# Performance work log

Measured on AMD Instinct MI355X. Metric: run time of the kernel, lower is better.

Reference implementation:

```python
import jax, jax.numpy as jnp
import numpy as np
from jax import lax

B, C, H, W = 2, 64, 128, 128
F_SCALE, STRIDE = 2, 2
F = F_SCALE * STRIDE            # pixel-unshuffle factor = 4
CK = C // 16                    # attention channel dim = 4
SCALE_DIM = C // F_SCALE        # softmax scale uses embed_size//f_scale = 32


def setup_inputs() -> dict:
    key = jax.random.key(0)
    ks = jax.random.split(key, 16)
    g = lambda i, shape, s=0.05: jax.random.normal(ks[i], shape, jnp.float32) * s
    return {
        "x":   jax.random.normal(ks[0], (B, C, H, W), jnp.float32),
        # conv1 = Sequential(1x1 C->CK, 1x1 CK->CK)
        "w1a": g(1, (CK, C)), "b1a": g(2, (CK,)),
        "w1b": g(3, (CK, CK)), "b1b": g(4, (CK,)),
        # wqk parameter (torch.randn, std 1)
        "wqk": jax.random.normal(ks[5], (CK, CK), jnp.float32),
        # conv2: 1x1 CK->C ; conv: 1x1 C->C
        "w2":  g(6, (C, CK)), "b2": g(7, (C,)),
        "wc":  g(8, (C, C)), "bc": g(9, (C,)),
        # FF (GridSANaive): 1x1 C->C/4, 3x3 dilated C/4->C/4, 1x1 C/4->C
        "wf1": g(10, (C // 4, C)), "bf1": g(11, (C // 4,)),
        "wf2": g(12, (C // 4, C // 4, 3, 3)), "bf2": g(13, (C // 4,)),
        "wf3": g(14, (C, C // 4)), "bf3": g(15, (C,)),
    }


def conv1x1(x, w, b):
    return jnp.einsum('bchw,oc->bohw', x, w) + b[None, :, None, None]


def grid_attention(x, wqk):
    b, c, h, w = x.shape
    sh = h // 2
    x = jnp.pad(x, ((0, 0), (0, 0), (sh, 0), (0, 0)))      # Shift2d pad (top)
    # F.layer_norm over last 3 dims, no affine, eps=1e-5
    mu = jnp.mean(x, axis=(1, 2, 3), keepdims=True)
    var = jnp.var(x, axis=(1, 2, 3), keepdims=True)
    xx = (x - mu) / jnp.sqrt(var + 1e-5)
    hh, ww = xx.shape[2], xx.shape[3]
    ph, pw = (F - hh % F) % F, (F - ww % F) % F
    xx = jnp.pad(xx, ((0, 0), (0, 0), (0, ph), (0, pw)))
    gh, gw = (hh + ph) // F, (ww + pw) // F
    # pixel_unshuffle: channel layout (c, fy, fx)
    xx = xx.reshape(b, c, gh, F, gw, F).transpose(0, 1, 3, 5, 2, 4)
    xx = xx.reshape(b, c * F * F, gh, gw)
    # rearrange 'b (f c) h w -> (b f) c h w', f=F*F (mixes layout, as in original)
    xx = xx.reshape(b * F * F, c, gh, gw)
    L = gh * gw
    tok = xx.transpose(0, 2, 3, 1).reshape(b * F * F, L, c)   # (bg, L, c)
    qk = tok @ wqk
    qk = qk / (jnp.linalg.norm(qk, axis=-1, keepdims=True) + 1e-8)
    attn = (jnp.einsum('blk,bmk->blm', qk, qk) + 1.0) / (SCALE_DIM ** 0.5)
    attn = jax.nn.softmax(attn, axis=-1)
    out = jnp.einsum('blm,bmc->blc', attn, tok)
    out = out.reshape(b * F * F, gh, gw, c).transpose(0, 3, 1, 2)
    out = out.reshape(b, F * F * c, gh, gw)
    # pixel_shuffle: channel layout (fy, fx, c)
    out = out.reshape(b, F, F, c, gh, gw).transpose(0, 3, 4, 1, 5, 2)
    out = out.reshape(b, c, gh * F, gw * F)
    out = out[:, :, :hh, :ww]                               # undo shuffle pad
    return out[:, :, :-sh, :] if sh > 0 else out            # Shift2d crop (bottom)


def ff(x, wf1, bf1, wf2, bf2, wf3, bf3):
    h1 = jax.nn.relu(conv1x1(x, wf1, bf1))
    k = 1 + (STRIDE // 2) * 2   # ShiftConv2d offset for 3x3, dilation=STRIDE
    hp = jnp.pad(h1, ((0, 0), (0, 0), (k, 0), (0, 0)))
    h2 = lax.conv_general_dilated(
        hp, wf2, (1, 1), ((STRIDE, STRIDE), (STRIDE, STRIDE)),
        rhs_dilation=(STRIDE, STRIDE),
        dimension_numbers=('NCHW', 'OIHW', 'NCHW'))
    h2 = jax.nn.relu((h2 + bf2[None, :, None, None])[:, :, :-k, :])
    return conv1x1(h2, wf3, bf3)


def reference(x, w1a, b1a, w1b, b1b, wqk, w2, b2, wc, bc,
              wf1, bf1, wf2, bf2, wf3, bf3):
    a = conv1x1(conv1x1(x, w1a, b1a), w1b, b1b)
    att = grid_attention(a, wqk)
    y = x + conv1x1(conv1x1(att, w2, b2), wc, bc)
    return y + ff(y, wf1, bf1, wf2, bf2, wf3, bf3)
```

## Files before the change

### kernel.cpp

```cpp
#include <hip/hip_runtime.h>
#include <math.h>

#define CHW  (64*16384)
#define ATT_SCALE 0.17677669529663687f

__global__ __launch_bounds__(256) void k1_a_stats(
    const float* __restrict__ x, const float* __restrict__ w1a,
    const float* __restrict__ b1a, const float* __restrict__ w1b,
    const float* __restrict__ b1b, float* __restrict__ a,
    float* __restrict__ statsbuf) {
  __shared__ float sA[256];
  __shared__ float sb1[4];
  __shared__ float pc[4][4][256];
  __shared__ float rs[64], rq[64];
  int tid = threadIdx.x;
  {
    int o = tid >> 6, c = tid & 63;
    float s = 0.f;
    #pragma unroll
    for (int k = 0; k < 4; ++k) s += w1b[o*4+k] * w1a[k*64+c];
    sA[tid] = s;
  }
  if (tid < 4) {
    float s = b1b[tid];
    #pragma unroll
    for (int k = 0; k < 4; ++k) s += w1b[tid*4+k] * b1a[k];
    sb1[tid] = s;
  }
  __syncthreads();
  int quad = tid & 15, cg = tid >> 4;
  int gq = blockIdx.x * 16 + quad;
  int bb = gq >> 12;
  int px0 = (gq & 4095) * 4;
  const float* xp = x + bb*CHW + (cg*4)*16384 + px0;
  float4 acc[4];
  #pragma unroll
  for (int o = 0; o < 4; ++o) acc[o] = make_float4(0.f,0.f,0.f,0.f);
  #pragma unroll
  for (int cc = 0; cc < 4; ++cc) {
    float4 xv = *(const float4*)(xp + cc*16384);
    int c = cg*4 + cc;
    #pragma unroll
    for (int o = 0; o < 4; ++o) {
      float w = sA[o*64+c];
      acc[o].x += w*xv.x; acc[o].y += w*xv.y; acc[o].z += w*xv.z; acc[o].w += w*xv.w;
    }
  }
  #pragma unroll
  for (int o = 0; o < 4; ++o) {
    pc[0][o][tid] = acc[o].x; pc[1][o][tid] = acc[o].y;
    pc[2][o][tid] = acc[o].z; pc[3][o][tid] = acc[o].w;
  }
  __syncthreads();
  if (tid < 64) {
    int q2 = tid & 15, o = tid >> 4;
    float sx=0.f, sy=0.f, sz=0.f, sw=0.f;
    #pragma unroll
    for (int g2 = 0; g2 < 16; ++g2) {
      int idx = g2*16 + q2;
      sx += pc[0][o][idx]; sy += pc[1][o][idx];
      sz += pc[2][o][idx]; sw += pc[3][o][idx];
    }
    float bv = sb1[o];
    sx += bv; sy += bv; sz += bv; sw += bv;
    int gq2 = blockIdx.x*16 + q2;
    int b2 = gq2 >> 12; int p0 = (gq2 & 4095)*4;
    *(float4*)(a + b2*4*16384 + o*16384 + p0) = make_float4(sx,sy,sz,sw);
    rs[tid] = sx+sy+sz+sw;
    rq[tid] = sx*sx+sy*sy+sz*sz+sw*sw;
  }
  __syncthreads();
  for (int s2 = 32; s2; s2 >>= 1) {
    if (tid < s2) { rs[tid] += rs[tid+s2]; rq[tid] += rq[tid+s2]; }
    __syncthreads();
  }
  if (tid == 0) { statsbuf[blockIdx.x*2] = rs[0]; statsbuf[blockIdx.x*2+1] = rq[0]; }
}

__device__ __forceinline__ float poly_exp(float d) {
  return 1.f + d*(1.f + d*(0.5f + d*(0.16666667f + d*0.04166667f)));
}
__global__ __launch_bounds__(512) void k3_attn(
    const float* __restrict__ a, const float* __restrict__ statsbuf,
    const float* __restrict__ wqk, float* __restrict__ att) {
  __shared__ float4 kq[1024];
  __shared__ float4 kt[1024];
  __shared__ float red[16][5][128];
  __shared__ float sred[8];
  int tid = threadIdx.x;
  int g = blockIdx.x >> 3, qb = blockIdx.x & 7;
  int b = g >> 4, u = (g >> 2) & 3, v = g & 3;

  if (tid < 256) {
    float2 p = ((const float2*)statsbuf)[b*256 + tid];
    float vs = p.x, vq = p.y;
    #pragma unroll
    for (int off = 32; off; off >>= 1) {
      vs += __shfl_down(vs, off); vq += __shfl_down(vq, off);
    }
    if ((tid & 63) == 0) { sred[tid>>6] = vs; sred[4 + (tid>>6)] = vq; }
  }
  __syncthreads();
  float mu  = (sred[0]+sred[1]+sred[2]+sred[3]) * (1.f/98304.f);
  float var = (sred[4]+sred[5]+sred[6]+sred[7]) * (1.f/98304.f) - mu*mu;
  float rsig = rsqrtf(var + 1e-5f);

  const float* ap = a + (b*4+u)*16384;
  for (int m = tid; m < 1024; m += 512) {
    int t = 512 + m;
    int i = t >> 5, j = m & 31;
    float4 tv = *(const float4*)(ap + (i*4 + v - 64)*128 + j*4);
    tv.x = (tv.x-mu)*rsig; tv.y = (tv.y-mu)*rsig;
    tv.z = (tv.z-mu)*rsig; tv.w = (tv.w-mu)*rsig;
    float q0 = tv.x*wqk[0] + tv.y*wqk[4] + tv.z*wqk[8]  + tv.w*wqk[12];
    float q1 = tv.x*wqk[1] + tv.y*wqk[5] + tv.z*wqk[9]  + tv.w*wqk[13];
    float q2 = tv.x*wqk[2] + tv.y*wqk[6] + tv.z*wqk[10] + tv.w*wqk[14];
    float q3 = tv.x*wqk[3] + tv.y*wqk[7] + tv.z*wqk[11] + tv.w*wqk[15];
    float inv = 1.f / (sqrtf(q0*q0 + q1*q1 + q2*q2 + q3*q3) + 1e-8f);
    kq[m] = make_float4(q0*inv, q1*inv, q2*inv, q3*inv);
    kt[m] = tv;
  }
  float z = -mu*rsig;
  float4 t0tv = make_float4(z, z, z, z);
  float p0 = z*(wqk[0] + wqk[4] + wqk[8]  + wqk[12]);
  float p1 = z*(wqk[1] + wqk[5] + wqk[9]  + wqk[13]);
  float p2 = z*(wqk[2] + wqk[6] + wqk[10] + wqk[14]);
  float p3 = z*(wqk[3] + wqk[7] + wqk[11] + wqk[15]);
  float inv0 = 1.f / (sqrtf(p0*p0 + p1*p1 + p2*p2 + p3*p3) + 1e-8f);
  float4 t0qk = make_float4(p0*inv0, p1*inv0, p2*inv0, p3*inv0);
  __syncthreads();

  if (qb >= 4) {
    int qi = tid & 31, s = tid >> 5;
    int t0 = (qb - 4)*128 + qi*4;
    float4 q[4];
    #pragma unroll
    for (int j = 0; j < 4; ++j) {
      float4 vq = kq[t0 + j];
      q[j] = make_float4(vq.x*ATT_SCALE, vq.y*ATT_SCALE, vq.z*ATT_SCALE, vq.w*ATT_SCALE);
    }
    float den[4] = {0.f,0.f,0.f,0.f};
    float4 ov[4];
    #pragma unroll
    for (int j = 0; j < 4; ++j) ov[j] = make_float4(0.f,0.f,0.f,0.f);
    if (s == 0) {
      #pragma unroll
      for (int j = 0; j < 4; ++j) {
        float d = q[j].x*t0qk.x + q[j].y*t0qk.y + q[j].z*t0qk.z + q[j].w*t0qk.w;
        float e = 512.f * poly_exp(d);
        den[j] += e;
        ov[j].x += e*t0tv.x; ov[j].y += e*t0tv.y; ov[j].z += e*t0tv.z; ov[j].w += e*t0tv.w;
      }
    }
    int m0 = s * 64;
    #pragma unroll 2
    for (int m = m0; m < m0 + 64; ++m) {
      float4 kk = kq[m];
      float4 tv = kt[m];
      #pragma unroll
      for (int j = 0; j < 4; ++j) {
        float d = q[j].x*kk.x + q[j].y*kk.y + q[j].z*kk.z + q[j].w*kk.w;
        float e = poly_exp(d);
        den[j] += e;
        ov[j].x += e*tv.x; ov[j].y += e*tv.y; ov[j].z += e*tv.z; ov[j].w += e*tv.w;
      }
    }
    #pragma unroll
    for (int j = 0; j < 4; ++j) {
      int key = j*32 + qi;
      red[s][0][key] = den[j];
      red[s][1][key] = ov[j].x; red[s][2][key] = ov[j].y;
      red[s][3][key] = ov[j].z; red[s][4][key] = ov[j].w;
    }
    __syncthreads();
    if (tid < 128) {
      int qi_r = tid & 31, j_r = tid >> 5;
      float dsum=0.f, ox=0.f, oy=0.f, oz=0.f, ow=0.f;
      #pragma unroll
      for (int ss = 0; ss < 16; ++ss) {
        dsum += red[ss][0][tid];
        ox += red[ss][1][tid]; oy += red[ss][2][tid];
        oz += red[ss][3][tid]; ow += red[ss][4][tid];
      }
      float inv = 1.f / dsum;
      int t = qb*128 + qi_r*4 + j_r;
      int i = t >> 5, j = t & 31;
      float* ap2 = att + b*4*16384 + (i*4+u)*128 + (j*4+v);
      ap2[0]     = ox*inv;
      ap2[16384] = oy*inv;
      ap2[32768] = oz*inv;
      ap2[49152] = ow*inv;
    }
  } else {
    float4 qs = make_float4(t0qk.x*ATT_SCALE, t0qk.y*ATT_SCALE,
                            t0qk.z*ATT_SCALE, t0qk.w*ATT_SCALE);
    float den = 0.f; float4 ov = make_float4(0.f,0.f,0.f,0.f);
    #pragma unroll
    for (int mm = 0; mm < 2; ++mm) {
      int m = tid*2 + mm;
      float4 kk = kq[m];
      float4 tv = kt[m];
      float d = qs.x*kk.x + qs.y*kk.y + qs.z*kk.z + qs.w*kk.w;
      float e = poly_exp(d);
      den += e;
      ov.x += e*tv.x; ov.y += e*tv.y; ov.z += e*tv.z; ov.w += e*tv.w;
    }
    if (tid == 0) {
      float d = qs.x*t0qk.x + qs.y*t0qk.y + qs.z*t0qk.z + qs.w*t0qk.w;
      float e = 512.f * poly_exp(d);
      den += e;
      ov.x += e*t0tv.x; ov.y += e*t0tv.y; ov.z += e*t0tv.z; ov.w += e*t0tv.w;
    }
    float* sc = &red[0][0][0];
    sc[tid]        = den;
    sc[512 + tid]  = ov.x;
    sc[1024 + tid] = ov.y;
    sc[1536 + tid] = ov.z;
    sc[2048 + tid] = ov.w;
    __syncthreads();
    for (int s2 = 256; s2; s2 >>= 1) {
      if (tid < s2) {
        sc[tid]        += sc[tid + s2];
        sc[512 + tid]  += sc[512 + tid + s2];
        sc[1024 + tid] += sc[1024 + tid + s2];
        sc[1536 + tid] += sc[1536 + tid + s2];
        sc[2048 + tid] += sc[2048 + tid + s2];
      }
      __syncthreads();
    }
    float invd = 1.f / sc[0];
    float res0 = sc[512]*invd, res1 = sc[1024]*invd,
          res2 = sc[1536]*invd, res3 = sc[2048]*invd;
    int comp = tid >> 7, tloc = tid & 127;
    int t = qb*128 + tloc;
    int i = t >> 5, j = t & 31;
    float val = (comp == 0) ? res0 : (comp == 1) ? res1 : (comp == 2) ? res2 : res3;
    att[b*4*16384 + comp*16384 + (i*4+u)*128 + (j*4+v)] = val;
  }
}

__global__ __launch_bounds__(512) void k46_row(
    const float* __restrict__ x, const float* __restrict__ att,
    const float* __restrict__ w2p, const float* __restrict__ b2p,
    const float* __restrict__ wcp, const float* __restrict__ bcp,
    const float* __restrict__ wf1, const float* __restrict__ bf1,
    const float* __restrict__ wf2, const float* __restrict__ bf2,
    const float* __restrict__ wf3, const float* __restrict__ bf3,
    float* __restrict__ yo) {
  __shared__ float sWf[64][4];
  __shared__ float sbf[64];
  __shared__ float sw1[1024];
  __shared__ float sb1[16];
  __shared__ float4 satt[4][32];
  __shared__ float4 ylds[64][32];
  __shared__ float sbuf[16][3][136];
  __shared__ float h2buf[128][21];
  int tid = threadIdx.x;
  int lid = (blockIdx.x & 7) * 32 + (blockIdx.x >> 3);
  int bb = lid >> 7, h = lid & 127;

  if (tid < 256) {
    int o = tid >> 2, k = tid & 3;
    float s = 0.f;
    for (int c = 0; c < 64; ++c) s += wcp[o*64+c] * w2p[c*4+k];
    sWf[o][k] = s;
  }
  if (tid < 64) {
    float s = bcp[tid];
    for (int c = 0; c < 64; ++c) s += wcp[tid*64+c] * b2p[c];
    sbf[tid] = s;
  }
  for (int i = tid; i < 1024; i += 512) sw1[i] = wf1[i];
  if (tid < 16) sb1[tid] = bf1[tid];
  for (int idx = tid; idx < 16*3*136; idx += 512) (&sbuf[0][0][0])[idx] = 0.f;

  int quad = tid & 31, og = tid >> 5;
  #pragma unroll 1
  for (int ri = 0; ri < 4; ++ri) {
    int row = (ri == 3) ? h : (h - 5 + 2*ri);
    bool valid = (row >= 0);
    __syncthreads();
    if (valid && tid < 128) {
      int k = tid >> 5, q2 = tid & 31;
      satt[k][q2] = *(const float4*)(att + bb*4*16384 + k*16384 + row*128 + q2*4);
    }
    __syncthreads();
    if (valid) {
      float4 a0 = satt[0][quad], a1 = satt[1][quad],
             a2 = satt[2][quad], a3 = satt[3][quad];
      const float* xp = x + bb*CHW + row*128 + quad*4;
      #pragma unroll
      for (int cc = 0; cc < 4; ++cc) {
        int c = og*4 + cc;
        float4 xv = *(const float4*)(xp + c*16384);
        float w0 = sWf[c][0], w1 = sWf[c][1], w2v = sWf[c][2], w3 = sWf[c][3];
        float bv = sbf[c];
        float4 yv;
        yv.x = xv.x + w0*a0.x + w1*a1.x + w2v*a2.x + w3*a3.x + bv;
        yv.y = xv.y + w0*a0.y + w1*a1.y + w2v*a2.y + w3*a3.y + bv;
        yv.z = xv.z + w0*a0.z + w1*a1.z + w2v*a2.z + w3*a3.z + bv;
        yv.w = xv.w + w0*a0.w + w1*a1.w + w2v*a2.w + w3*a3.w + bv;
        ylds[c][quad] = yv;
      }
    }
    __syncthreads();
    if (valid && ri < 3) {
      float bv = sb1[og];
      float4 acc = make_float4(bv, bv, bv, bv);
      #pragma unroll 8
      for (int c = 0; c < 64; ++c) {
        float4 yv = ylds[c][quad];
        float wa = sw1[og*64+c];
        acc.x += wa*yv.x; acc.y += wa*yv.y; acc.z += wa*yv.z; acc.w += wa*yv.w;
      }
      int col = 4 + quad*4;
      sbuf[og][ri][col]   = fmaxf(acc.x, 0.f);
      sbuf[og][ri][col+1] = fmaxf(acc.y, 0.f);
      sbuf[og][ri][col+2] = fmaxf(acc.z, 0.f);
      sbuf[og][ri][col+3] = fmaxf(acc.w, 0.f);
    }
  }
  __syncthreads();

  int w = tid & 127;
  int g = __builtin_amdgcn_readfirstlane(tid >> 7);
  float acc[4];
  #pragma unroll
  for (int o = 0; o < 4; ++o) acc[o] = bf2[g*4+o];
  #pragma unroll 4
  for (int c = 0; c < 16; ++c) {
    #pragma unroll
    for (int r = 0; r < 3; ++r) {
      float tm2 = sbuf[c][r][w+2];
      float t00 = sbuf[c][r][w+4];
      float tp2 = sbuf[c][r][w+6];
      #pragma unroll
      for (int o = 0; o < 4; ++o) {
        const float* wp = wf2 + (((g*4+o)*16 + c)*3 + r)*3;
        acc[o] += wp[0]*tm2 + wp[1]*t00 + wp[2]*tp2;
      }
    }
  }
  #pragma unroll
  for (int o = 0; o < 4; ++o) h2buf[w][g*4+o] = fmaxf(acc[o], 0.f);
  __syncthreads();
  float hv[16];
  #pragma unroll
  for (int k = 0; k < 16; ++k) hv[k] = h2buf[w][k];
  const float* yrow = (const float*)ylds;
  float* ybase = yo + bb*CHW + h*128 + w;
  #pragma unroll 4
  for (int oc = 0; oc < 16; ++oc) {
    int o = g*16 + oc;
    float sv = bf3[o] + yrow[o*128 + w];
    #pragma unroll
    for (int k = 0; k < 16; ++k) sv += wf3[o*16+k]*hv[k];
    ybase[o*16384] = sv;
  }
}

extern "C" void kernel_launch(void* const* d_in, const int* in_sizes, int n_in,
                              void* d_out, int out_size, void* d_ws, size_t ws_size,
                              hipStream_t stream) {
  (void)in_sizes; (void)n_in; (void)out_size; (void)ws_size;
  const float* x   = (const float*)d_in[0];
  const float* w1a = (const float*)d_in[1];
  const float* b1a = (const float*)d_in[2];
  const float* w1b = (const float*)d_in[3];
  const float* b1b = (const float*)d_in[4];
  const float* wqk = (const float*)d_in[5];
  const float* w2  = (const float*)d_in[6];
  const float* b2  = (const float*)d_in[7];
  const float* wc  = (const float*)d_in[8];
  const float* bc  = (const float*)d_in[9];
  const float* wf1 = (const float*)d_in[10];
  const float* bf1 = (const float*)d_in[11];
  const float* wf2 = (const float*)d_in[12];
  const float* bf2 = (const float*)d_in[13];
  const float* wf3 = (const float*)d_in[14];
  const float* bf3 = (const float*)d_in[15];

  float* ws = (float*)d_ws;
  float*  a_    = ws;
  float*  stats = ws + 131072;
  float*  att   = ws + 525312;

  k1_a_stats<<<512, 256, 0, stream>>>(x, w1a, b1a, w1b, b1b, a_, stats);
  k3_attn   <<<256, 512, 0, stream>>>(a_, stats, wqk, att);
  k46_row   <<<256, 512, 0, stream>>>(x, att, w2, b2, wc, bc, wf1, bf1,
                                      wf2, bf2, wf3, bf3, (float*)d_out);
}
```

Baseline: 130.4 us.

## Rebalance attention blocks so every block does equal real-query work

The attention kernel previously split blocks unevenly: half computed real-token queries over 16 key slices, and the other half computed the identical padded-row output with a deep tree reduction. Now all 8 blocks per group take 64 real queries each, split across 32 key slices of 32 keys. Block 0 additionally computes the padded-row constant using wave shuffles instead of the shared-memory tree. The intent is to remove load imbalance and the costly repeated reductions, at the cost of a larger 32-way final reduction done by only 64 threads.

```diff
diff --git a/kernel.cpp b/kernel.cpp
--- a/kernel.cpp
+++ b/kernel.cpp
@@ -85,8 +85,9 @@
     const float* __restrict__ wqk, float* __restrict__ att) {
   __shared__ float4 kq[1024];
   __shared__ float4 kt[1024];
-  __shared__ float red[16][5][128];
+  __shared__ float red[32][328];
   __shared__ float sred[8];
+  __shared__ float padred[8][5];
   int tid = threadIdx.x;
   int g = blockIdx.x >> 3, qb = blockIdx.x & 7;
   int b = g >> 4, u = (g >> 2) & 3, v = g & 3;
@@ -130,71 +131,52 @@
   float4 t0qk = make_float4(p0*inv0, p1*inv0, p2*inv0, p3*inv0);
   __syncthreads();
 
-  if (qb >= 4) {
-    int qi = tid & 31, s = tid >> 5;
-    int t0 = (qb - 4)*128 + qi*4;
-    float4 q[4];
+  int qi = tid & 15, s = tid >> 4;
+  int t0k = qb*64 + qi*4;
+  float4 q[4];
+  #pragma unroll
+  for (int j = 0; j < 4; ++j) {
+    float4 vq = kq[t0k + j];
+    q[j] = make_float4(vq.x*ATT_SCALE, vq.y*ATT_SCALE, vq.z*ATT_SCALE, vq.w*ATT_SCALE);
+  }
+  float den[4] = {0.f,0.f,0.f,0.f};
+  float4 ov[4];
+  #pragma unroll
+  for (int j = 0; j < 4; ++j) ov[j] = make_float4(0.f,0.f,0.f,0.f);
+  if (s == 0) {
     #pragma unroll
     for (int j = 0; j < 4; ++j) {
-      float4 vq = kq[t0 + j];
-      q[j] = make_float4(vq.x*ATT_SCALE, vq.y*ATT_SCALE, vq.z*ATT_SCALE, vq.w*ATT_SCALE);
-    }
-    float den[4] = {0.f,0.f,0.f,0.f};
-    float4 ov[4];
-    #pragma unroll
-    for (int j = 0; j < 4; ++j) ov[j] = make_float4(0.f,0.f,0.f,0.f);
-    if (s == 0) {
-      #pragma unroll
-      for (int j = 0; j < 4; ++j) {
-        float d = q[j].x*t0qk.x + q[j].y*t0qk.y + q[j].z*t0qk.z + q[j].w*t0qk.w;
-        float e = 512.f * poly_exp(d);
-        den[j] += e;
-        ov[j].x += e*t0tv.x; ov[j].y += e*t0tv.y; ov[j].z += e*t0tv.z; ov[j].w += e*t0tv.w;
-      }
-    }
-    int m0 = s * 64;
-    #pragma unroll 2
-    for (int m = m0; m < m0 + 64; ++m) {
-      float4 kk = kq[m];
-      float4 tv = kt[m];
-      #pragma unroll
-      for (int j = 0; j < 4; ++j) {
-        float d = q[j].x*kk.x + q[j].y*kk.y + q[j].z*kk.z + q[j].w*kk.w;
-        float e = poly_exp(d);
-        den[j] += e;
-        ov[j].x += e*tv.x; ov[j].y += e*tv.y; ov[j].z += e*tv.z; ov[j].w += e*tv.w;
-      }
-    }
+      float d = q[j].x*t0qk.x + q[j].y*t0qk.y + q[j].z*t0qk.z + q[j].w*t0qk.w;
+      float e = 512.f * poly_exp(d);
+      den[j] += e;
+      ov[j].x += e*t0tv.x; ov[j].y += e*t0tv.y; ov[j].z += e*t0tv.z; ov[j].w += e*t0tv.w;
+    }
+  }
+  int m0 = s * 32;
+  #pragma unroll 2
+  for (int m = m0; m < m0 + 32; ++m) {
+    float4 kk = kq[m];
+    float4 tv = kt[m];
     #pragma unroll
     for (int j = 0; j < 4; ++j) {
-      int key = j*32 + qi;
-      red[s][0][key] = den[j];
-      red[s][1][key] = ov[j].x; red[s][2][key] = ov[j].y;
-      red[s][3][key] = ov[j].z; red[s][4][key] = ov[j].w;
-    }
-    __syncthreads();
-    if (tid < 128) {
-      int qi_r = tid & 31, j_r = tid >> 5;
-      float dsum=0.f, ox=0.f, oy=0.f, oz=0.f, ow=0.f;
-      #pragma unroll
-      for (int ss = 0; ss < 16; ++ss) {
-        dsum += red[ss][0][tid];
-        ox += red[ss][1][tid]; oy += red[ss][2][tid];
-        oz += red[ss][3][tid]; ow += red[ss][4][tid];
-      }
-      float inv = 1.f / dsum;
-      int t = qb*128 + qi_r*4 + j_r;
-      int i = t >> 5, j = t & 31;
-      float* ap2 = att + b*4*16384 + (i*4+u)*128 + (j*4+v);
-      ap2[0]     = ox*inv;
-      ap2[16384] = oy*inv;
-      ap2[32768] = oz*inv;
-      ap2[49152] = ow*inv;
-    }
-  } else {
+      float d = q[j].x*kk.x + q[j].y*kk.y + q[j].z*kk.z + q[j].w*kk.w;
+      float e = poly_exp(d);
+      den[j] += e;
+      ov[j].x += e*tv.x; ov[j].y += e*tv.y; ov[j].z += e*tv.z; ov[j].w += e*tv.w;
+    }
+  }
+  #pragma unroll
+  for (int j = 0; j < 4; ++j) {
+    int key = j*16 + qi;
+    red[s][0*64+key] = den[j];
+    red[s][1*64+key] = ov[j].x; red[s][2*64+key] = ov[j].y;
+    red[s][3*64+key] = ov[j].z; red[s][4*64+key] = ov[j].w;
+  }
+
+  if (qb == 0) {
     float4 qs = make_float4(t0qk.x*ATT_SCALE, t0qk.y*ATT_SCALE,
                             t0qk.z*ATT_SCALE, t0qk.w*ATT_SCALE);
-    float den = 0.f; float4 ov = make_float4(0.f,0.f,0.f,0.f);
+    float pden = 0.f; float4 pov = make_float4(0.f,0.f,0.f,0.f);
     #pragma unroll
     for (int mm = 0; mm < 2; ++mm) {
       int m = tid*2 + mm;
@@ -202,40 +184,65 @@
       float4 tv = kt[m];
       float d = qs.x*kk.x + qs.y*kk.y + qs.z*kk.z + qs.w*kk.w;
       float e = poly_exp(d);
-      den += e;
-      ov.x += e*tv.x; ov.y += e*tv.y; ov.z += e*tv.z; ov.w += e*tv.w;
+      pden += e;
+      pov.x += e*tv.x; pov.y += e*tv.y; pov.z += e*tv.z; pov.w += e*tv.w;
     }
     if (tid == 0) {
       float d = qs.x*t0qk.x + qs.y*t0qk.y + qs.z*t0qk.z + qs.w*t0qk.w;
       float e = 512.f * poly_exp(d);
-      den += e;
-      ov.x += e*t0tv.x; ov.y += e*t0tv.y; ov.z += e*t0tv.z; ov.w += e*t0tv.w;
-    }
-    float* sc = &red[0][0][0];
-    sc[tid]        = den;
-    sc[512 + tid]  = ov.x;
-    sc[1024 + tid] = ov.y;
-    sc[1536 + tid] = ov.z;
-    sc[2048 + tid] = ov.w;
-    __syncthreads();
-    for (int s2 = 256; s2; s2 >>= 1) {
-      if (tid < s2) {
-        sc[tid]        += sc[tid + s2];
-        sc[512 + tid]  += sc[512 + tid + s2];
-        sc[1024 + tid] += sc[1024 + tid + s2];
-        sc[1536 + tid] += sc[1536 + tid + s2];
-        sc[2048 + tid] += sc[2048 + tid + s2];
-      }
-      __syncthreads();
-    }
-    float invd = 1.f / sc[0];
-    float res0 = sc[512]*invd, res1 = sc[1024]*invd,
-          res2 = sc[1536]*invd, res3 = sc[2048]*invd;
-    int comp = tid >> 7, tloc = tid & 127;
-    int t = qb*128 + tloc;
+      pden += e;
+      pov.x += e*t0tv.x; pov.y += e*t0tv.y; pov.z += e*t0tv.z; pov.w += e*t0tv.w;
+    }
+    #pragma unroll
+    for (int off = 32; off; off >>= 1) {
+      pden  += __shfl_down(pden,  off);
+      pov.x += __shfl_down(pov.x, off); pov.y += __shfl_down(pov.y, off);
+      pov.z += __shfl_down(pov.z, off); pov.w += __shfl_down(pov.w, off);
+    }
+    if ((tid & 63) == 0) {
+      int wv = tid >> 6;
+      padred[wv][0] = pden;
+      padred[wv][1] = pov.x; padred[wv][2] = pov.y;
+      padred[wv][3] = pov.z; padred[wv][4] = pov.w;
+    }
+  }
+  __syncthreads();
+
+  if (tid < 64) {
+    float dsum=0.f, ox=0.f, oy=0.f, oz=0.f, ow=0.f;
+    #pragma unroll 8
+    for (int ss = 0; ss < 32; ++ss) {
+      dsum += red[ss][0*64+tid];
+      ox += red[ss][1*64+tid]; oy += red[ss][2*64+tid];
+      oz += red[ss][3*64+tid]; ow += red[ss][4*64+tid];
+    }
+    float inv = 1.f / dsum;
+    int qi_r = tid & 15, j_r = tid >> 4;
+    int t = 512 + qb*64 + qi_r*4 + j_r;
     int i = t >> 5, j = t & 31;
-    float val = (comp == 0) ? res0 : (comp == 1) ? res1 : (comp == 2) ? res2 : res3;
-    att[b*4*16384 + comp*16384 + (i*4+u)*128 + (j*4+v)] = val;
+    float* ap2 = att + b*4*16384 + (i*4+u)*128 + (j*4+v);
+    ap2[0]     = ox*inv;
+    ap2[16384] = oy*inv;
+    ap2[32768] = oz*inv;
+    ap2[49152] = ow*inv;
+  }
+
+  if (qb == 0) {
+    float dsum = padred[0][0]+padred[1][0]+padred[2][0]+padred[3][0]
+               + padred[4][0]+padred[5][0]+padred[6][0]+padred[7][0];
+    float invd = 1.f / dsum;
+    float res[4];
+    #pragma unroll
+    for (int c = 0; c < 4; ++c)
+      res[c] = (padred[0][c+1]+padred[1][c+1]+padred[2][c+1]+padred[3][c+1]
+              + padred[4][c+1]+padred[5][c+1]+padred[6][c+1]+padred[7][c+1]) * invd;
+    int t = tid;
+    int i = t >> 5, j = t & 31;
+    float* ap2 = att + b*4*16384 + (i*4+u)*128 + (j*4+v);
+    ap2[0]     = res[0];
+    ap2[16384] = res[1];
+    ap2[32768] = res[2];
+    ap2[49152] = res[3];
   }
 }
 
```

Result: faster. 126.5 us, median of 2 (-3.0%).
